# Optimization experiments

Hardware: AMD Instinct MI355X
Metric: run time of the kernel (lower is better)

Reference implementation:

```python
import jax, jax.numpy as jnp
import numpy as np

WS = 7
NH = 4

def _rel_idx(ws):
    ch, cw = np.meshgrid(np.arange(ws), np.arange(ws), indexing='ij')
    cf = np.stack([ch.ravel(), cw.ravel()])  # [2, ws*ws]
    rel = cf[:, :, None] - cf[:, None, :]
    rel = rel.transpose(1, 2, 0)
    rel[:, :, 0] += ws - 1
    rel[:, :, 1] += ws - 1
    rel[:, :, 0] *= 2 * ws - 1
    return jnp.asarray(rel.sum(-1), dtype=jnp.int32)  # [N, N]

def layernorm(x, g, b, eps=1e-5):
    m = jnp.mean(x, -1, keepdims=True)
    v = jnp.var(x, -1, keepdims=True)
    return (x - m) * jax.lax.rsqrt(v + eps) * g + b

def setup_inputs() -> dict:
    key = jax.random.key(0)
    ks = jax.random.split(key, 8)
    B, HH, WW, C = 32, 56, 56, 128
    hid = 512
    s = 0.02
    return {
        'x': jax.random.normal(ks[0], (B, HH * WW, C), jnp.float32),
        'H': HH, 'W': WW,
        'norm1_g': jnp.ones((C,), jnp.float32),
        'norm1_b': jnp.zeros((C,), jnp.float32),
        'qkv_w': jax.random.normal(ks[1], (3 * C, C), jnp.float32) * s,
        'qkv_b': jnp.zeros((3 * C,), jnp.float32),
        'rel_bias_table': jax.random.normal(ks[2], ((2 * WS - 1) ** 2, NH), jnp.float32) * s,
        'rel_idx': _rel_idx(WS),
        'proj_w': jax.random.normal(ks[3], (C, C), jnp.float32) * s,
        'proj_b': jnp.zeros((C,), jnp.float32),
        'norm2_g': jnp.ones((C,), jnp.float32),
        'norm2_b': jnp.zeros((C,), jnp.float32),
        'mlp_w1': jax.random.normal(ks[4], (hid, C), jnp.float32) * s,
        'mlp_b1': jnp.zeros((hid,), jnp.float32),
        'mlp_w2': jax.random.normal(ks[5], (C, hid), jnp.float32) * s,
        'mlp_b2': jnp.zeros((C,), jnp.float32),
    }

def swin_block(x, H, W, norm1_g, norm1_b, qkv_w, qkv_b, rel_bias_table, rel_idx,
               proj_w, proj_b, norm2_g, norm2_b, mlp_w1, mlp_b1, mlp_w2, mlp_b2,
               shift=3, ws=WS, nh=NH):
    B, L, C = x.shape
    N = ws * ws
    hd = C // nh
    scale = hd ** -0.5
    shortcut = x
    h = layernorm(x, norm1_g, norm1_b).reshape(B, H, W, C)
    if shift > 0:
        h = jnp.roll(h, (-shift, -shift), axis=(1, 2))
    # window partition -> [B*nW, N, C]
    h = h.reshape(B, H // ws, ws, W // ws, ws, C).transpose(0, 1, 3, 2, 4, 5).reshape(-1, N, C)
    # attention (no mask in source forward)
    qkv = h @ qkv_w.T + qkv_b  # [B_, N, 3C]
    qkv = qkv.reshape(-1, N, 3, nh, hd).transpose(2, 0, 3, 1, 4)
    q, k, v = qkv[0] * scale, qkv[1], qkv[2]  # [B_, nh, N, hd]
    attn = jnp.einsum('bhnd,bhmd->bhnm', q, k)
    bias = rel_bias_table[rel_idx.reshape(-1)].reshape(N, N, nh).transpose(2, 0, 1)
    attn = jax.nn.softmax(attn + bias[None], axis=-1)
    o = jnp.einsum('bhnm,bhmd->bhnd', attn, v).transpose(0, 2, 1, 3).reshape(-1, N, C)
    o = o @ proj_w.T + proj_b
    # window reverse -> [B, H, W, C]
    o = o.reshape(B, H // ws, W // ws, ws, ws, C).transpose(0, 1, 3, 2, 4, 5).reshape(B, H, W, C)
    if shift > 0:
        o = jnp.roll(o, (shift, shift), axis=(1, 2))
    x = shortcut + o.reshape(B, L, C)
    h2 = layernorm(x, norm2_g, norm2_b)
    h2 = jax.nn.gelu(h2 @ mlp_w1.T + mlp_b1, approximate=False) @ mlp_w2.T + mlp_b2
    return x + h2

def reference(x, H, W, norm1_g, norm1_b, qkv_w, qkv_b, rel_bias_table, rel_idx,
              proj_w, proj_b, norm2_g, norm2_b, mlp_w1, mlp_b1, mlp_w2, mlp_b2):
    return swin_block(x, H, W, norm1_g, norm1_b, qkv_w, qkv_b, rel_bias_table, rel_idx,
                      proj_w, proj_b, norm2_g, norm2_b, mlp_w1, mlp_b1, mlp_w2, mlp_b2)
```

## Files before the change

kernel.cpp:

```cpp
#include <hip/hip_runtime.h>
#include <hip/hip_bf16.h>


#define NWIN 2048

typedef short short8  __attribute__((ext_vector_type(8)));
typedef short short4v __attribute__((ext_vector_type(4)));
typedef float f32x4   __attribute__((ext_vector_type(4)));

union Frag { int i[4]; unsigned u[4]; short8 s; };

#define QKVW_OFF  0
#define PROJW_OFF 49152
#define W1_OFF    65536
#define W2_OFF    131072
#define BIAS_BYTE_OFF 393216

__device__ __forceinline__ short f2bs(float v) {
  __hip_bfloat16 h = __float2bfloat16(v);
  union { __hip_bfloat16 h; short s; } u; u.h = h; return u.s;
}
__device__ __forceinline__ float gelu_f(float v) {
  float u = v * (0.7978845608028654f + 0.03567740814f * v * v);
  return v * __builtin_amdgcn_rcpf(1.f + __expf(-2.f * u));
}

__global__ __launch_bounds__(256) void conv_kernel(
    const float* __restrict__ qkvw, const float* __restrict__ projw,
    const float* __restrict__ w1,   const float* __restrict__ w2,
    const float* __restrict__ tab,  const int* __restrict__ ridx,
    __hip_bfloat16* __restrict__ wsb, float* __restrict__ biasT)
{
  int idx = blockIdx.x * 256 + threadIdx.x;
  if (idx < 49152)       wsb[QKVW_OFF + idx]          = __float2bfloat16(qkvw[idx]);
  else if (idx < 65536)  wsb[PROJW_OFF + idx - 49152] = __float2bfloat16(projw[idx - 49152]);
  else if (idx < 131072) wsb[W1_OFF + idx - 65536]    = __float2bfloat16(w1[idx - 65536]);
  else if (idx < 196608) wsb[W2_OFF + idx - 131072]   = __float2bfloat16(w2[idx - 131072]);
  else if (idx < 212992) {
    int i = idx - 196608;
    int h = i >> 12, m = (i >> 6) & 63, n = i & 63;
    biasT[i] = (m < 49 && n < 49) ? tab[ridx[n*49 + m]*4 + h] : 0.f;
  }
}

__global__ __launch_bounds__(512, 4) void fused_kernel(
    const float* __restrict__ x,
    const float* __restrict__ n1g, const float* __restrict__ n1b,
    const __hip_bfloat16* __restrict__ qkvwb, const float* __restrict__ qkvb,
    const float* __restrict__ biasT,
    const __hip_bfloat16* __restrict__ projwb, const float* __restrict__ projb,
    const float* __restrict__ n2g, const float* __restrict__ n2b,
    const __hip_bfloat16* __restrict__ w1b, const float* __restrict__ b1,
    const __hip_bfloat16* __restrict__ w2b, const float* __restrict__ b2,
    float* __restrict__ out)
{
  __shared__ alignas(16) __hip_bfloat16 hbuf[64][136];
  __shared__ alignas(16) char shmem[36864];
  __hip_bfloat16* const Kl  = (__hip_bfloat16*)shmem;
  __hip_bfloat16* const vTl = (__hip_bfloat16*)(shmem + 20480);
  float*          const x2s = (float*)shmem;
  __hip_bfloat16* const hbA = (__hip_bfloat16*)shmem;
  __hip_bfloat16* const hbB = (__hip_bfloat16*)(shmem + 17408);

  const int tid = threadIdx.x, wave = tid >> 6, lane = tid & 63;
  const int l15 = lane & 15, quad = lane >> 4;
  const int h = wave >> 1, half = wave & 1;
  const int b = blockIdx.x >> 6, wi = (blockIdx.x >> 3) & 7, wj = blockIdx.x & 7;

  {
    float g0 = n1g[lane], g1 = n1g[lane+64], e0 = n1b[lane], e1 = n1b[lane+64];
    float va[7], vb[7];
    #pragma unroll
    for (int i = 0; i < 7; ++i) {
      int n = wave + i*8;
      va[i] = 0.f; vb[i] = 0.f;
      if (n < 49) {
        int r = n / 7, c = n - r * 7;
        int si = wi*7 + r + 3; if (si >= 56) si -= 56;
        int sj = wj*7 + c + 3; if (sj >= 56) sj -= 56;
        const float* xr = x + (b*3136 + si*56 + sj) * 128;
        va[i] = xr[lane]; vb[i] = xr[lane + 64];
      }
    }
    #pragma unroll
    for (int i = 0; i < 7; ++i) {
      int n = wave + i*8;
      if (n < 49) {
        float s = va[i] + vb[i], sq = va[i]*va[i] + vb[i]*vb[i];
        #pragma unroll
        for (int off = 32; off > 0; off >>= 1) {
          s  += __shfl_xor(s,  off);
          sq += __shfl_xor(sq, off);
        }
        float mean = s * 0.0078125f;
        float var  = sq * 0.0078125f - mean*mean;
        float rstd = rsqrtf(var + 1e-5f);
        hbuf[n][lane]    = __float2bfloat16((va[i]-mean)*rstd*g0 + e0);
        hbuf[n][lane+64] = __float2bfloat16((vb[i]-mean)*rstd*g1 + e1);
      }
    }
  }
  __syncthreads();

  {
    f32x4 kacc[4] = {}, vacc[4] = {};
    #pragma unroll
    for (int ks = 0; ks < 4; ++ks) {
      short8 hf[4];
      #pragma unroll
      for (int mt = 0; mt < 4; ++mt)
        hf[mt] = *(const short8*)(&hbuf[mt*16 + l15][ks*32 + quad*8]);
      short8 wfk = *(const short8*)(qkvwb + (128 + wave*16 + l15)*128 + ks*32 + quad*8);
      short8 wfv = *(const short8*)(qkvwb + (256 + wave*16 + l15)*128 + ks*32 + quad*8);
      #pragma unroll
      for (int mt = 0; mt < 4; ++mt) {
        kacc[mt] = __builtin_amdgcn_mfma_f32_16x16x32_bf16(wfk, hf[mt], kacc[mt], 0, 0, 0);
        vacc[mt] = __builtin_amdgcn_mfma_f32_16x16x32_bf16(hf[mt], wfv, vacc[mt], 0, 0, 0);
      }
    }
    {
      const int fo = wave*16 + quad*4;
      const int hh = wave >> 1, d0 = fo & 31;
      float bb[4];
      #pragma unroll
      for (int r = 0; r < 4; ++r) bb[r] = qkvb[128 + fo + r];
      #pragma unroll
      for (int mt = 0; mt < 4; ++mt) {
        int m = mt*16 + l15;
        if (m < 49) {
          short4v pkv;
          #pragma unroll
          for (int r = 0; r < 4; ++r) pkv[r] = f2bs(kacc[mt][r] + bb[r]);
          *(short4v*)(Kl + (hh*64 + m)*40 + d0) = pkv;
        }
      }
    }
    {
      const int fv = wave*16 + l15;
      const int hh = wave >> 1, d = fv & 31;
      const float bia = qkvb[256 + fv];
      #pragma unroll
      for (int mt = 0; mt < 4; ++mt) {
        int m0 = mt*16 + quad*4;
        #pragma unroll
        for (int r = 0; r < 4; ++r) {
          int m = m0 + r;
          float v = (m < 49) ? (vacc[mt][r] + bia) : 0.f;
          vTl[(hh*32 + d)*64 + ((((m>>3) ^ (d & 7))) << 3) + (m & 7)] = __float2bfloat16(v);
        }
      }
    }
  }

  Frag qfr[2];
  {
    f32x4 qacc[2][2] = {};
    #pragma unroll
    for (int ks = 0; ks < 4; ++ks) {
      short8 hfq[2];
      #pragma unroll
      for (int nt = 0; nt < 2; ++nt)
        hfq[nt] = *(const short8*)(&hbuf[(half*2 + nt)*16 + l15][ks*32 + quad*8]);
      #pragma unroll
      for (int tq = 0; tq < 2; ++tq) {
        short8 wf = *(const short8*)(qkvwb + ((h*2 + tq)*16 + l15)*128 + ks*32 + quad*8);
        #pragma unroll
        for (int nt = 0; nt < 2; ++nt)
          qacc[tq][nt] = __builtin_amdgcn_mfma_f32_16x16x32_bf16(wf, hfq[nt], qacc[tq][nt], 0, 0, 0);
      }
    }
    const float qs = 0.17677669529663687f;
    unsigned pkq[2][2][2];
    #pragma unroll
    for (int tq = 0; tq < 2; ++tq) {
      float bb[4];
      #pragma unroll
      for (int r = 0; r < 4; ++r) bb[r] = qkvb[h*32 + tq*16 + quad*4 + r];
      #pragma unroll
      for (int nt = 0; nt < 2; ++nt)
        #pragma unroll
        for (int i = 0; i < 2; ++i) {
          unsigned lo = (unsigned short)f2bs((qacc[tq][nt][2*i]   + bb[2*i])   * qs);
          unsigned hi = (unsigned short)f2bs((qacc[tq][nt][2*i+1] + bb[2*i+1]) * qs);
          pkq[tq][nt][i] = lo | (hi << 16);
        }
    }
    #pragma unroll
    for (int nt = 0; nt < 2; ++nt)
      #pragma unroll
      for (int p = 0; p < 4; ++p) {
        int sl = (((quad & 1)*2 + (p >> 1)) << 4) | l15;
        int a  = __shfl((int)pkq[0][nt][p & 1], sl);
        int c2 = __shfl((int)pkq[1][nt][p & 1], sl);
        qfr[nt].i[p] = (quad >= 2) ? c2 : a;
      }
  }
  __syncthreads();

  {
    short8 kf[4];
    #pragma unroll
    for (int mt = 0; mt < 4; ++mt)
      kf[mt] = *(const short8*)(Kl + (h*64 + mt*16 + l15)*40 + quad*8);

    f32x4 sacc[4][2] = {};
    #pragma unroll
    for (int mt = 0; mt < 4; ++mt)
      #pragma unroll
      for (int nc = 0; nc < 2; ++nc)
        sacc[mt][nc] = __builtin_amdgcn_mfma_f32_16x16x32_bf16(kf[mt], qfr[nc].s, sacc[mt][nc], 0, 0, 0);

    const float* bT = biasT + h*4096;
    #pragma unroll
    for (int mt = 0; mt < 4; ++mt)
      #pragma unroll
      for (int nc = 0; nc < 2; ++nc)
        #pragma unroll
        for (int r = 0; r < 4; ++r)
          sacc[mt][nc][r] += bT[(mt*16 + quad*4 + r)*64 + (half*2 + nc)*16 + l15];

    unsigned pk[4][2][2];
    #pragma unroll
    for (int nc = 0; nc < 2; ++nc) {
      float mx = -1e30f;
      #pragma unroll
      for (int mt = 0; mt < 3; ++mt)
        #pragma unroll
        for (int r = 0; r < 4; ++r) mx = fmaxf(mx, sacc[mt][nc][r]);
      mx = fmaxf(mx, (quad == 0) ? sacc[3][nc][0] : -1e30f);
      mx = fmaxf(mx, __shfl_xor(mx, 16));
      mx = fmaxf(mx, __shfl_xor(mx, 32));
      float sum = 0.f;
      #pragma unroll
      for (int mt = 0; mt < 3; ++mt)
        #pragma unroll
        for (int r = 0; r < 4; ++r) {
          float e = __expf(sacc[mt][nc][r] - mx);
          sacc[mt][nc][r] = e; sum += e;
        }
      {
        float e = (quad == 0) ? __expf(sacc[3][nc][0] - mx) : 0.f;
        sacc[3][nc][0] = e; sacc[3][nc][1] = 0.f; sacc[3][nc][2] = 0.f; sacc[3][nc][3] = 0.f;
        sum += e;
      }
      sum += __shfl_xor(sum, 16);
      sum += __shfl_xor(sum, 32);
      float inv = 1.f / sum;
      #pragma unroll
      for (int mt = 0; mt < 4; ++mt)
        #pragma unroll
        for (int i = 0; i < 2; ++i) {
          unsigned lo = (unsigned short)f2bs(sacc[mt][nc][2*i]   * inv);
          unsigned hi = (unsigned short)f2bs(sacc[mt][nc][2*i+1] * inv);
          pk[mt][nc][i] = lo | (hi << 16);
        }
    }
    Frag pfr[2][2];
    #pragma unroll
    for (int kt = 0; kt < 2; ++kt)
      #pragma unroll
      for (int nc = 0; nc < 2; ++nc)
        #pragma unroll
        for (int p = 0; p < 4; ++p) {
          int sl = (((quad & 1)*2 + (p >> 1)) << 4) | l15;
          int a  = __shfl((int)pk[kt*2    ][nc][p & 1], sl);
          int c2 = __shfl((int)pk[kt*2 + 1][nc][p & 1], sl);
          pfr[kt][nc].i[p] = (quad >= 2) ? c2 : a;
        }

    f32x4 oacc[2][2] = {};
    #pragma unroll
    for (int kt = 0; kt < 2; ++kt) {
      short8 vf[2];
      #pragma unroll
      for (int dt = 0; dt < 2; ++dt)
        vf[dt] = *(const short8*)(vTl + (h*32 + dt*16 + l15)*64 + (((kt*4 + quad) ^ (l15 & 7)) << 3));
      #pragma unroll
      for (int dt = 0; dt < 2; ++dt)
        #pragma unroll
        for (int nc = 0; nc < 2; ++nc)
          oacc[dt][nc] = __builtin_amdgcn_mfma_f32_16x16x32_bf16(vf[dt], pfr[kt][nc].s, oacc[dt][nc], 0, 0, 0);
    }
    #pragma unroll
    for (int dt = 0; dt < 2; ++dt)
      #pragma unroll
      for (int nc = 0; nc < 2; ++nc) {
        int n = (half*2 + nc)*16 + l15;
        if (n < 49) {
          short4v pkv;
          #pragma unroll
          for (int r = 0; r < 4; ++r) pkv[r] = f2bs(oacc[dt][nc][r]);
          *(short4v*)(&hbuf[n][h*32 + dt*16 + quad*4]) = pkv;
        }
      }
  }
  __syncthreads();

  f32x4 x2v[4];
  {
    const int n = wave * 16 + l15;
    float xres[4][4];
    #pragma unroll
    for (int mt = 0; mt < 4; ++mt) {
      #pragma unroll
      for (int r = 0; r < 4; ++r) {
        int m = mt*16 + quad*4 + r;
        float v = 0.f;
        if (m < 49) {
          int rr = m / 7, cc = m - rr * 7;
          int si = wi*7 + rr + 3; if (si >= 56) si -= 56;
          int sj = wj*7 + cc + 3; if (sj >= 56) sj -= 56;
          v = x[(b*3136 + si*56 + sj) * 128 + n];
        }
        xres[mt][r] = v;
      }
    }
    f32x4 acc[4] = {};
    #pragma unroll
    for (int ks = 0; ks < 4; ++ks) {
      short8 af[4];
      #pragma unroll
      for (int mt = 0; mt < 4; ++mt)
        af[mt] = *(const short8*)(&hbuf[mt*16 + l15][ks*32 + quad*8]);
      short8 bfr = *(const short8*)(projwb + n*128 + ks*32 + quad*8);
      #pragma unroll
      for (int mt = 0; mt < 4; ++mt)
        acc[mt] = __builtin_amdgcn_mfma_f32_16x16x32_bf16(af[mt], bfr, acc[mt], 0, 0, 0);
    }
    float pbv = projb[n];
    #pragma unroll
    for (int mt = 0; mt < 4; ++mt) {
      #pragma unroll
      for (int r = 0; r < 4; ++r) {
        int m = mt*16 + quad*4 + r;
        float v = 0.f;
        if (m < 49) v = acc[mt][r] + pbv + xres[mt][r];
        x2v[mt][r] = v;
        x2s[m*132 + n] = v;
      }
    }
  }
  __syncthreads();

  {
    float g0 = n2g[lane], g1 = n2g[lane+64], e0 = n2b[lane], e1 = n2b[lane+64];
    for (int n = wave; n < 49; n += 8) {
      float v0 = x2s[n*132 + lane], v1 = x2s[n*132 + lane + 64];
      float s = v0 + v1, sq = v0*v0 + v1*v1;
      #pragma unroll
      for (int off = 32; off > 0; off >>= 1) {
        s  += __shfl_xor(s,  off);
        sq += __shfl_xor(sq, off);
      }
      float mean = s * 0.0078125f;
      float var  = sq * 0.0078125f - mean*mean;
      float rstd = rsqrtf(var + 1e-5f);
      hbuf[n][lane]    = __float2bfloat16((v0-mean)*rstd*g0 + e0);
      hbuf[n][lane+64] = __float2bfloat16((v1-mean)*rstd*g1 + e1);
    }
    __hip_bfloat16 z = __float2bfloat16(0.f);
    for (int n = 49 + wave; n < 64; n += 8) {
      hbuf[n][lane] = z; hbuf[n][lane+64] = z;
    }
  }
  __syncthreads();

  f32x4 acc2[4] = {};
  const int fb2 = wave * 16;

  auto G1 = [&](int c, __hip_bfloat16* dst) {
    const int jg = c*128 + wave*16;
    f32x4 a1[4] = {};
    #pragma unroll
    for (int ks = 0; ks < 4; ++ks) {
      short8 lf[4];
      #pragma unroll
      for (int mt = 0; mt < 4; ++mt)
        lf[mt] = *(const short8*)(&hbuf[mt*16 + l15][ks*32 + quad*8]);
      short8 wf = *(const short8*)(w1b + (jg + l15)*128 + ks*32 + quad*8);
      #pragma unroll
      for (int mt = 0; mt < 4; ++mt)
        a1[mt] = __builtin_amdgcn_mfma_f32_16x16x32_bf16(wf, lf[mt], a1[mt], 0, 0, 0);
    }
    float bb[4];
    #pragma unroll
    for (int r = 0; r < 4; ++r) bb[r] = b1[jg + quad*4 + r];
    #pragma unroll
    for (int mt = 0; mt < 4; ++mt) {
      int m = mt*16 + l15;
      short4v pkv;
      #pragma unroll
      for (int r = 0; r < 4; ++r) pkv[r] = f2bs(gelu_f(a1[mt][r] + bb[r]));
      *(short4v*)(dst + m*136 + wave*16 + quad*4) = pkv;
    }
  };
  auto G2 = [&](int c, const __hip_bfloat16* src) {
    #pragma unroll
    for (int ks = 0; ks < 4; ++ks) {
      short8 af[4];
      #pragma unroll
      for (int mt = 0; mt < 4; ++mt)
        af[mt] = *(const short8*)(src + (mt*16 + l15)*136 + ks*32 + quad*8);
      short8 wf = *(const short8*)(w2b + (fb2 + l15)*512 + c*128 + ks*32 + quad*8);
      #pragma unroll
      for (int mt = 0; mt < 4; ++mt)
        acc2[mt] = __builtin_amdgcn_mfma_f32_16x16x32_bf16(af[mt], wf, acc2[mt], 0, 0, 0);
    }
  };

  G1(0, hbA);
  __syncthreads();
  G1(1, hbB); G2(0, hbA);
  __syncthreads();
  G1(2, hbA); G2(1, hbB);
  __syncthreads();
  G1(3, hbB); G2(2, hbA);
  __syncthreads();
  G2(3, hbB);

  {
    const int f = fb2 + l15;
    const float bb = b2[f];
    #pragma unroll
    for (int mt = 0; mt < 4; ++mt) {
      #pragma unroll
      for (int r = 0; r < 4; ++r) {
        int m = mt*16 + quad*4 + r;
        if (m < 49) {
          int rr = m / 7, cc = m - rr * 7;
          int si = wi*7 + rr + 3; if (si >= 56) si -= 56;
          int sj = wj*7 + cc + 3; if (sj >= 56) sj -= 56;
          int o = (b*3136 + si*56 + sj) * 128 + f;
          out[o] = acc2[mt][r] + bb + x2v[mt][r];
        }
      }
    }
  }
}

extern "C" void kernel_launch(void* const* d_in, const int* in_sizes, int n_in,
                              void* d_out, int out_size, void* d_ws, size_t ws_size,
                              hipStream_t stream) {
  const float* x     = (const float*)d_in[0];
  const float* n1g   = (const float*)d_in[3];
  const float* n1b   = (const float*)d_in[4];
  const float* qkvw  = (const float*)d_in[5];
  const float* qkvb  = (const float*)d_in[6];
  const float* tab   = (const float*)d_in[7];
  const int*   ridx  = (const int*)d_in[8];
  const float* projw = (const float*)d_in[9];
  const float* projb = (const float*)d_in[10];
  const float* n2g   = (const float*)d_in[11];
  const float* n2b   = (const float*)d_in[12];
  const float* w1    = (const float*)d_in[13];
  const float* b1    = (const float*)d_in[14];
  const float* w2    = (const float*)d_in[15];
  const float* b2    = (const float*)d_in[16];
  float* outp = (float*)d_out;

  __hip_bfloat16* wsb = (__hip_bfloat16*)d_ws;
  float* biasT = (float*)((char*)d_ws + BIAS_BYTE_OFF);

  hipLaunchKernelGGL(conv_kernel, dim3(832), dim3(256), 0, stream,
                     qkvw, projw, w1, w2, tab, ridx, wsb, biasT);
  hipLaunchKernelGGL(fused_kernel, dim3(NWIN), dim3(512), 0, stream,
                     x, n1g, n1b, wsb + QKVW_OFF, qkvb, biasT, wsb + PROJW_OFF, projb,
                     n2g, n2b, wsb + W1_OFF, b1, wsb + W2_OFF, b2, outp);
}
```

Before: 259.1 us.

## Restructure MLP into two 256-wide chunks with single buffer, pad V transpose layout

The MLP hidden dimension is now processed in two 256-wide chunks through a single shared buffer, replacing four 128-wide chunks double-buffered across two buffers. Each wave computes two 16-row weight tiles per step, so every loaded hidden-state fragment feeds more MFMAs. The price is serialized G1/G2 phases with no overlap between chunks, plus slightly more LDS. Separately, the transposed V buffer switches from an XOR-swizzled layout to a padded row stride with vectorized 4-element stores. The relative-position bias loads are also hoisted ahead of the QK MFMAs to hide their latency.

```diff
diff --git a/kernel.cpp b/kernel.cpp
--- a/kernel.cpp
+++ b/kernel.cpp
@@ -55,12 +55,11 @@
     float* __restrict__ out)
 {
   __shared__ alignas(16) __hip_bfloat16 hbuf[64][136];
-  __shared__ alignas(16) char shmem[36864];
+  __shared__ alignas(16) char shmem[38912];
   __hip_bfloat16* const Kl  = (__hip_bfloat16*)shmem;
   __hip_bfloat16* const vTl = (__hip_bfloat16*)(shmem + 20480);
   float*          const x2s = (float*)shmem;
-  __hip_bfloat16* const hbA = (__hip_bfloat16*)shmem;
-  __hip_bfloat16* const hbB = (__hip_bfloat16*)(shmem + 17408);
+  __hip_bfloat16* const hb  = (__hip_bfloat16*)shmem;
 
   const int tid = threadIdx.x, wave = tid >> 6, lane = tid & 63;
   const int l15 = lane & 15, quad = lane >> 4;
@@ -142,12 +141,13 @@
       #pragma unroll
       for (int mt = 0; mt < 4; ++mt) {
         int m0 = mt*16 + quad*4;
+        short4v pkv;
         #pragma unroll
         for (int r = 0; r < 4; ++r) {
-          int m = m0 + r;
-          float v = (m < 49) ? (vacc[mt][r] + bia) : 0.f;
-          vTl[(hh*32 + d)*64 + ((((m>>3) ^ (d & 7))) << 3) + (m & 7)] = __float2bfloat16(v);
-        }
+          float v = (m0 + r < 49) ? (vacc[mt][r] + bia) : 0.f;
+          pkv[r] = f2bs(v);
+        }
+        *(short4v*)(vTl + (hh*32 + d)*72 + m0) = pkv;
       }
     }
   }
@@ -198,6 +198,16 @@
   __syncthreads();
 
   {
+    const float* bT = biasT + h*4096;
+    float bv[4][2][4];
+    #pragma unroll
+    for (int mt = 0; mt < 4; ++mt)
+      #pragma unroll
+      for (int nc = 0; nc < 2; ++nc)
+        #pragma unroll
+        for (int r = 0; r < 4; ++r)
+          bv[mt][nc][r] = bT[(mt*16 + quad*4 + r)*64 + (half*2 + nc)*16 + l15];
+
     short8 kf[4];
     #pragma unroll
     for (int mt = 0; mt < 4; ++mt)
@@ -210,14 +220,13 @@
       for (int nc = 0; nc < 2; ++nc)
         sacc[mt][nc] = __builtin_amdgcn_mfma_f32_16x16x32_bf16(kf[mt], qfr[nc].s, sacc[mt][nc], 0, 0, 0);
 
-    const float* bT = biasT + h*4096;
     #pragma unroll
     for (int mt = 0; mt < 4; ++mt)
       #pragma unroll
       for (int nc = 0; nc < 2; ++nc)
         #pragma unroll
         for (int r = 0; r < 4; ++r)
-          sacc[mt][nc][r] += bT[(mt*16 + quad*4 + r)*64 + (half*2 + nc)*16 + l15];
+          sacc[mt][nc][r] += bv[mt][nc][r];
 
     unsigned pk[4][2][2];
     #pragma unroll
@@ -274,7 +283,7 @@
       short8 vf[2];
       #pragma unroll
       for (int dt = 0; dt < 2; ++dt)
-        vf[dt] = *(const short8*)(vTl + (h*32 + dt*16 + l15)*64 + (((kt*4 + quad) ^ (l15 & 7)) << 3));
+        vf[dt] = *(const short8*)(vTl + (h*32 + dt*16 + l15)*72 + kt*32 + quad*8);
       #pragma unroll
       for (int dt = 0; dt < 2; ++dt)
         #pragma unroll
@@ -368,55 +377,60 @@
   f32x4 acc2[4] = {};
   const int fb2 = wave * 16;
 
-  auto G1 = [&](int c, __hip_bfloat16* dst) {
-    const int jg = c*128 + wave*16;
-    f32x4 a1[4] = {};
+  auto G1 = [&](int c) {
+    const int jbl = wave * 32;
+    f32x4 acc1[2][4] = {};
     #pragma unroll
     for (int ks = 0; ks < 4; ++ks) {
       short8 lf[4];
       #pragma unroll
       for (int mt = 0; mt < 4; ++mt)
         lf[mt] = *(const short8*)(&hbuf[mt*16 + l15][ks*32 + quad*8]);
-      short8 wf = *(const short8*)(w1b + (jg + l15)*128 + ks*32 + quad*8);
-      #pragma unroll
-      for (int mt = 0; mt < 4; ++mt)
-        a1[mt] = __builtin_amdgcn_mfma_f32_16x16x32_bf16(wf, lf[mt], a1[mt], 0, 0, 0);
-    }
-    float bb[4];
-    #pragma unroll
-    for (int r = 0; r < 4; ++r) bb[r] = b1[jg + quad*4 + r];
-    #pragma unroll
-    for (int mt = 0; mt < 4; ++mt) {
-      int m = mt*16 + l15;
-      short4v pkv;
-      #pragma unroll
-      for (int r = 0; r < 4; ++r) pkv[r] = f2bs(gelu_f(a1[mt][r] + bb[r]));
-      *(short4v*)(dst + m*136 + wave*16 + quad*4) = pkv;
+      #pragma unroll
+      for (int jt = 0; jt < 2; ++jt) {
+        short8 wf = *(const short8*)(w1b + (c*256 + jbl + jt*16 + l15)*128 + ks*32 + quad*8);
+        #pragma unroll
+        for (int mt = 0; mt < 4; ++mt)
+          acc1[jt][mt] = __builtin_amdgcn_mfma_f32_16x16x32_bf16(wf, lf[mt], acc1[jt][mt], 0, 0, 0);
+      }
+    }
+    #pragma unroll
+    for (int jt = 0; jt < 2; ++jt) {
+      int j0l = jbl + jt*16 + quad*4;
+      float bb[4];
+      #pragma unroll
+      for (int r = 0; r < 4; ++r) bb[r] = b1[c*256 + j0l + r];
+      #pragma unroll
+      for (int mt = 0; mt < 4; ++mt) {
+        int m = mt*16 + l15;
+        short4v pkv;
+        #pragma unroll
+        for (int r = 0; r < 4; ++r) pkv[r] = f2bs(gelu_f(acc1[jt][mt][r] + bb[r]));
+        *(short4v*)(hb + m*264 + j0l) = pkv;
+      }
     }
   };
-  auto G2 = [&](int c, const __hip_bfloat16* src) {
-    #pragma unroll
-    for (int ks = 0; ks < 4; ++ks) {
+  auto G2 = [&](int c) {
+    #pragma unroll
+    for (int ks = 0; ks < 8; ++ks) {
       short8 af[4];
       #pragma unroll
       for (int mt = 0; mt < 4; ++mt)
-        af[mt] = *(const short8*)(src + (mt*16 + l15)*136 + ks*32 + quad*8);
-      short8 wf = *(const short8*)(w2b + (fb2 + l15)*512 + c*128 + ks*32 + quad*8);
+        af[mt] = *(const short8*)(hb + (mt*16 + l15)*264 + ks*32 + quad*8);
+      short8 wf = *(const short8*)(w2b + (fb2 + l15)*512 + c*256 + ks*32 + quad*8);
       #pragma unroll
       for (int mt = 0; mt < 4; ++mt)
         acc2[mt] = __builtin_amdgcn_mfma_f32_16x16x32_bf16(af[mt], wf, acc2[mt], 0, 0, 0);
     }
   };
 
-  G1(0, hbA);
-  __syncthreads();
-  G1(1, hbB); G2(0, hbA);
-  __syncthreads();
-  G1(2, hbA); G2(1, hbB);
-  __syncthreads();
-  G1(3, hbB); G2(2, hbA);
-  __syncthreads();
-  G2(3, hbB);
+  G1(0);
+  __syncthreads();
+  G2(0);
+  __syncthreads();
+  G1(1);
+  __syncthreads();
+  G2(1);
 
   {
     const int f = fb2 + l15;
```

Result: slower. 272.5 us (+5.2%).
